# Performance work log

Measured on AMD Instinct MI355X. Metric: run time of the kernel, lower is better.

## Reference

```python
import jax, jax.numpy as jnp
import numpy as np

B, H, W, Z = 4, 256, 256, 64
ITERATIONS = 8
EPSILON = 1e-06
CENTER = 6.0  # 7-point Laplacian diagonal


def _stencil(x):
    # x: [B, H, W, Z]; zero (Dirichlet) boundaries via padded shifts
    west = jnp.pad(x[:, :, :-1, :], ((0, 0), (0, 0), (1, 0), (0, 0)))
    east = jnp.pad(x[:, :, 1:, :], ((0, 0), (0, 0), (0, 1), (0, 0)))
    north = jnp.pad(x[:, :-1, :, :], ((0, 0), (1, 0), (0, 0), (0, 0)))
    south = jnp.pad(x[:, 1:, :, :], ((0, 0), (0, 1), (0, 0), (0, 0)))
    bottom = jnp.pad(x[:, :, :, :-1], ((0, 0), (0, 0), (0, 0), (1, 0)))
    top = jnp.pad(x[:, :, :, 1:], ((0, 0), (0, 0), (0, 0), (0, 1)))
    return CENTER * x - west - east - south - north - bottom - top


def _dot(a, b):
    # per-sample dot product, keepdims for scalar broadcast
    return jnp.sum(a * b, axis=(1, 2, 3), keepdims=True)


def setup_inputs() -> dict:
    key = jax.random.key(0)
    k1, k2, k3 = jax.random.split(key, 3)
    shape = (B, H, W, Z)
    return {
        "x": jax.random.normal(k1, shape, dtype=jnp.float32),
        "b": jax.random.normal(k2, shape, dtype=jnp.float32),
        "reference_sol": jax.random.normal(k3, shape, dtype=jnp.float32),
    }


def reference(x, b, reference_sol):
    r = b - _stencil(x)
    p = r
    rho = _dot(r, r)

    def body(carry, _):
        x, r, p, rho = carry
        w = _stencil(p)
        eta = _dot(p, w)
        alpha = rho / (eta + EPSILON)
        x = x + alpha * p
        r = r - alpha * w
        rho_next = _dot(r, r)
        beta = rho_next / (rho + EPSILON)
        p = r + beta * p
        return (x, r, p, rho_next), None

    (x, r, p, rho), _ = jax.lax.scan(body, (x, r, p, rho), None, length=ITERATIONS)

    diff = x - reference_sol
    loss = jnp.mean(diff * diff)
    max_error = jnp.max(jnp.abs(diff))
    residual_norm_sq = jnp.mean(rho)
    return (loss, x, max_error, residual_norm_sq)
```

## Files before the change

### kernel.cpp

```cpp
#include <hip/hip_runtime.h>

#define B_ 4
#define H_ 256
#define W_ 256
#define Z_ 64
#define NB_ (H_*W_*Z_)
#define N_  (B_*NB_)
#define ITER_ 8
#define EPS_ 1e-6f
#define SLOTS_ 64

#define RHO_OFF   0
#define ETA_OFF   ((ITER_+1)*B_*SLOTS_)
#define LOSS_OFF  (ETA_OFF + ITER_*B_*SLOTS_)
#define MAXE_OFF  (LOSS_OFF + SLOTS_)
#define SCAL_FLOATS (MAXE_OFF + SLOTS_)

struct F8 { float4 a, b; };

__device__ __forceinline__ float wsum(float v){
  v += __shfl_xor(v,32); v += __shfl_xor(v,16); v += __shfl_xor(v,8);
  v += __shfl_xor(v,4);  v += __shfl_xor(v,2);  v += __shfl_xor(v,1);
  return v;
}
__device__ __forceinline__ float wmaxr(float v){
  v = fmaxf(v,__shfl_xor(v,32)); v = fmaxf(v,__shfl_xor(v,16));
  v = fmaxf(v,__shfl_xor(v,8));  v = fmaxf(v,__shfl_xor(v,4));
  v = fmaxf(v,__shfl_xor(v,2));  v = fmaxf(v,__shfl_xor(v,1));
  return v;
}
__device__ __forceinline__ float read_sum(const float* s){
  return wsum(s[threadIdx.x & 63]);
}
__device__ __forceinline__ void block_atomic_sum(float v, float* dst, float* lds){
  v = wsum(v);
  int wid = threadIdx.x >> 6, lane = threadIdx.x & 63;
  if (lane == 0) lds[wid] = v;
  __syncthreads();
  if (threadIdx.x == 0) atomicAdd(dst, lds[0]+lds[1]+lds[2]+lds[3]);
}

__device__ __forceinline__ float4 ld4(const float* p){ return *(const float4*)p; }

__device__ __forceinline__ void sub8(F8& s, const F8& n){
  s.a.x-=n.a.x; s.a.y-=n.a.y; s.a.z-=n.a.z; s.a.w-=n.a.w;
  s.b.x-=n.b.x; s.b.y-=n.b.y; s.b.z-=n.b.z; s.b.w-=n.b.w;
}

__device__ __forceinline__ void zcore(const F8& c, int zc, F8& st){
  float zl = __shfl_up(c.b.w, 1);
  float zr = __shfl_down(c.a.x, 1);
  zl = (zc > 0) ? zl : 0.f;
  zr = (zc < 7) ? zr : 0.f;
  st.a.x = 6.f*c.a.x - zl    - c.a.y;
  st.a.y = 6.f*c.a.y - c.a.x - c.a.z;
  st.a.z = 6.f*c.a.z - c.a.y - c.a.w;
  st.a.w = 6.f*c.a.w - c.a.z - c.b.x;
  st.b.x = 6.f*c.b.x - c.a.w - c.b.y;
  st.b.y = 6.f*c.b.y - c.b.x - c.b.z;
  st.b.z = 6.f*c.b.z - c.b.y - c.b.w;
  st.b.w = 6.f*c.b.w - c.b.z - zr;
}

__device__ __forceinline__ void stencil1_2(const float* __restrict__ a, int base0,
                                           int w, int h0, int zc,
                                           F8& c0, F8& c1, F8& st0, F8& st1)
{
  const int base1 = base0 + W_*Z_;
  c0.a = ld4(a+base0); c0.b = ld4(a+base0+4);
  c1.a = ld4(a+base1); c1.b = ld4(a+base1+4);
  zcore(c0, zc, st0);
  zcore(c1, zc, st1);
  F8 t;
  if (w > 0)    { t.a = ld4(a+base0-Z_); t.b = ld4(a+base0-Z_+4); sub8(st0,t);
                  t.a = ld4(a+base1-Z_); t.b = ld4(a+base1-Z_+4); sub8(st1,t); }
  if (w < W_-1) { t.a = ld4(a+base0+Z_); t.b = ld4(a+base0+Z_+4); sub8(st0,t);
                  t.a = ld4(a+base1+Z_); t.b = ld4(a+base1+Z_+4); sub8(st1,t); }
  if (h0 > 0)   { t.a = ld4(a+base0-W_*Z_); t.b = ld4(a+base0-W_*Z_+4); sub8(st0,t); }
  sub8(st0, c1);
  sub8(st1, c0);
  if (h0 < H_-2){ t.a = ld4(a+base1+W_*Z_); t.b = ld4(a+base1+W_*Z_+4); sub8(st1,t); }
}

__device__ __forceinline__ F8 comb8(const float* r, const float* p, float beta, int idx){
  F8 o;
  float4 ra = ld4(r+idx), rb = ld4(r+idx+4);
  float4 pa = ld4(p+idx), pb = ld4(p+idx+4);
  o.a.x = ra.x + beta*pa.x; o.a.y = ra.y + beta*pa.y;
  o.a.z = ra.z + beta*pa.z; o.a.w = ra.w + beta*pa.w;
  o.b.x = rb.x + beta*pb.x; o.b.y = rb.y + beta*pb.y;
  o.b.z = rb.z + beta*pb.z; o.b.w = rb.w + beta*pb.w;
  return o;
}
__device__ __forceinline__ void stencil2_2(const float* __restrict__ r,
                                           const float* __restrict__ p, float beta,
                                           int base0, int w, int h0, int zc,
                                           F8& c0, F8& c1, F8& st0, F8& st1)
{
  const int base1 = base0 + W_*Z_;
  c0 = comb8(r,p,beta,base0);
  c1 = comb8(r,p,beta,base1);
  zcore(c0, zc, st0);
  zcore(c1, zc, st1);
  if (w > 0)    { sub8(st0, comb8(r,p,beta,base0-Z_));
                  sub8(st1, comb8(r,p,beta,base1-Z_)); }
  if (w < W_-1) { sub8(st0, comb8(r,p,beta,base0+Z_));
                  sub8(st1, comb8(r,p,beta,base1+Z_)); }
  if (h0 > 0)   sub8(st0, comb8(r,p,beta,base0-W_*Z_));
  sub8(st0, c1);
  sub8(st1, c0);
  if (h0 < H_-2) sub8(st1, comb8(r,p,beta,base1+W_*Z_));
}

__device__ __forceinline__ float dot8(const F8& a, const F8& b){
  return a.a.x*b.a.x + a.a.y*b.a.y + a.a.z*b.a.z + a.a.w*b.a.w
       + a.b.x*b.b.x + a.b.y*b.b.y + a.b.z*b.b.z + a.b.w*b.b.w;
}

#define IDX2_SETUP \
  const int zc = threadIdx.x & 7; \
  const int wl = threadIdx.x >> 3; \
  const int w  = blockIdx.x*32 + wl; \
  const int h0 = blockIdx.y*2; \
  const int bb = blockIdx.z; \
  const int base0 = ((bb*H_ + h0)*W_ + w)*Z_ + zc*8; \
  const int flat = (blockIdx.z*gridDim.y + blockIdx.y)*gridDim.x + blockIdx.x; \
  const int slot = flat & (SLOTS_-1);

__global__ __launch_bounds__(256) void k_init2(const float* __restrict__ x,
                                               const float* __restrict__ b,
                                               float* __restrict__ r,
                                               float* scal)
{
  __shared__ float lds[4];
  IDX2_SETUP
  const int base1 = base0 + W_*Z_;
  F8 c0,c1,st0,st1;
  stencil1_2(x, base0, w, h0, zc, c0, c1, st0, st1);
  float4 b0 = ld4(b+base0), b1 = ld4(b+base0+4);
  float4 b2 = ld4(b+base1), b3 = ld4(b+base1+4);
  F8 rv0, rv1;
  rv0.a = make_float4(b0.x-st0.a.x, b0.y-st0.a.y, b0.z-st0.a.z, b0.w-st0.a.w);
  rv0.b = make_float4(b1.x-st0.b.x, b1.y-st0.b.y, b1.z-st0.b.z, b1.w-st0.b.w);
  rv1.a = make_float4(b2.x-st1.a.x, b2.y-st1.a.y, b2.z-st1.a.z, b2.w-st1.a.w);
  rv1.b = make_float4(b3.x-st1.b.x, b3.y-st1.b.y, b3.z-st1.b.z, b3.w-st1.b.w);
  *(float4*)(r+base0)   = rv0.a;
  *(float4*)(r+base0+4) = rv0.b;
  *(float4*)(r+base1)   = rv1.a;
  *(float4*)(r+base1+4) = rv1.b;
  block_atomic_sum(dot8(rv0,rv0)+dot8(rv1,rv1),
                   scal + RHO_OFF + (0*B_+bb)*SLOTS_ + slot, lds);
}

__global__ __launch_bounds__(256) void k_a0_2(const float* __restrict__ r,
                                              float* __restrict__ pnew,
                                              float* scal)
{
  __shared__ float lds[4];
  IDX2_SETUP
  const int base1 = base0 + W_*Z_;
  F8 c0,c1,st0,st1;
  stencil1_2(r, base0, w, h0, zc, c0, c1, st0, st1);
  if (pnew) {
    *(float4*)(pnew+base0)   = c0.a; *(float4*)(pnew+base0+4) = c0.b;
    *(float4*)(pnew+base1)   = c1.a; *(float4*)(pnew+base1+4) = c1.b;
  }
  block_atomic_sum(dot8(c0,st0)+dot8(c1,st1),
                   scal + ETA_OFF + (0*B_+bb)*SLOTS_ + slot, lds);
}

__global__ __launch_bounds__(256) void k_a2(const float* __restrict__ r,
                                            const float* __restrict__ pold,
                                            float* __restrict__ pnew,
                                            float* scal, int it)
{
  __shared__ float lds[4];
  IDX2_SETUP
  const int base1 = base0 + W_*Z_;
  float num = read_sum(scal + RHO_OFF + (it*B_+bb)*SLOTS_);
  float den = read_sum(scal + RHO_OFF + ((it-1)*B_+bb)*SLOTS_);
  float beta = num / (den + EPS_);
  F8 c0,c1,st0,st1;
  stencil2_2(r, pold, beta, base0, w, h0, zc, c0, c1, st0, st1);
  *(float4*)(pnew+base0)   = c0.a;
  *(float4*)(pnew+base0+4) = c0.b;
  *(float4*)(pnew+base1)   = c1.a;
  *(float4*)(pnew+base1+4) = c1.b;
  block_atomic_sum(dot8(c0,st0)+dot8(c1,st1),
                   scal + ETA_OFF + (it*B_+bb)*SLOTS_ + slot, lds);
}

__global__ __launch_bounds__(256) void k_b2(float* __restrict__ x,
                                            const float* r_in,
                                            float* r_out,
                                            const float* p,
                                            float* scal, int it)
{
  __shared__ float lds[4];
  IDX2_SETUP
  const int base1 = base0 + W_*Z_;
  float num = read_sum(scal + RHO_OFF + (it*B_+bb)*SLOTS_);
  float den = read_sum(scal + ETA_OFF + (it*B_+bb)*SLOTS_);
  float alpha = num / (den + EPS_);
  F8 c0,c1,st0,st1;
  stencil1_2(p, base0, w, h0, zc, c0, c1, st0, st1);
  float rho = 0.f;
  {
    float4 x0 = ld4(x+base0), x1 = ld4(x+base0+4);
    x0.x += alpha*c0.a.x; x0.y += alpha*c0.a.y; x0.z += alpha*c0.a.z; x0.w += alpha*c0.a.w;
    x1.x += alpha*c0.b.x; x1.y += alpha*c0.b.y; x1.z += alpha*c0.b.z; x1.w += alpha*c0.b.w;
    *(float4*)(x+base0)   = x0;
    *(float4*)(x+base0+4) = x1;
    float4 r0 = ld4(r_in+base0), r1 = ld4(r_in+base0+4);
    r0.x -= alpha*st0.a.x; r0.y -= alpha*st0.a.y; r0.z -= alpha*st0.a.z; r0.w -= alpha*st0.a.w;
    r1.x -= alpha*st0.b.x; r1.y -= alpha*st0.b.y; r1.z -= alpha*st0.b.z; r1.w -= alpha*st0.b.w;
    *(float4*)(r_out+base0)   = r0;
    *(float4*)(r_out+base0+4) = r1;
    rho += r0.x*r0.x + r0.y*r0.y + r0.z*r0.z + r0.w*r0.w
         + r1.x*r1.x + r1.y*r1.y + r1.z*r1.z + r1.w*r1.w;
  }
  {
    float4 x0 = ld4(x+base1), x1 = ld4(x+base1+4);
    x0.x += alpha*c1.a.x; x0.y += alpha*c1.a.y; x0.z += alpha*c1.a.z; x0.w += alpha*c1.a.w;
    x1.x += alpha*c1.b.x; x1.y += alpha*c1.b.y; x1.z += alpha*c1.b.z; x1.w += alpha*c1.b.w;
    *(float4*)(x+base1)   = x0;
    *(float4*)(x+base1+4) = x1;
    float4 r0 = ld4(r_in+base1), r1 = ld4(r_in+base1+4);
    r0.x -= alpha*st1.a.x; r0.y -= alpha*st1.a.y; r0.z -= alpha*st1.a.z; r0.w -= alpha*st1.a.w;
    r1.x -= alpha*st1.b.x; r1.y -= alpha*st1.b.y; r1.z -= alpha*st1.b.z; r1.w -= alpha*st1.b.w;
    *(float4*)(r_out+base1)   = r0;
    *(float4*)(r_out+base1+4) = r1;
    rho += r0.x*r0.x + r0.y*r0.y + r0.z*r0.z + r0.w*r0.w
         + r1.x*r1.x + r1.y*r1.y + r1.z*r1.z + r1.w*r1.w;
  }
  block_atomic_sum(rho, scal + RHO_OFF + ((it+1)*B_+bb)*SLOTS_ + slot, lds);
}

__device__ __forceinline__ void sten_core_o(const F8& c, const F8& wm, const F8& wp,
                                            const F8& hm, const F8& hp,
                                            float zl, float zr, F8& st)
{
  st.a.x = 6.f*c.a.x - wm.a.x - wp.a.x - hm.a.x - hp.a.x - zl     - c.a.y;
  st.a.y = 6.f*c.a.y - wm.a.y - wp.a.y - hm.a.y - hp.a.y - c.a.x  - c.a.z;
  st.a.z = 6.f*c.a.z - wm.a.z - wp.a.z - hm.a.z - hp.a.z - c.a.y  - c.a.w;
  st.a.w = 6.f*c.a.w - wm.a.w - wp.a.w - hm.a.w - hp.a.w - c.a.z  - c.b.x;
  st.b.x = 6.f*c.b.x - wm.b.x - wp.b.x - hm.b.x - hp.b.x - c.a.w  - c.b.y;
  st.b.y = 6.f*c.b.y - wm.b.y - wp.b.y - hm.b.y - hp.b.y - c.b.x  - c.b.z;
  st.b.z = 6.f*c.b.z - wm.b.z - wp.b.z - hm.b.z - hp.b.z - c.b.y  - c.b.w;
  st.b.w = 6.f*c.b.w - wm.b.w - wp.b.w - hm.b.w - hp.b.w - c.b.z  - zr;
}
__device__ __forceinline__ void stencil1_o(const float* __restrict__ a, int base,
                                           int w, int h, int zc, F8& c, F8& st)
{
  c.a = ld4(a+base); c.b = ld4(a+base+4);
  F8 zero; zero.a = make_float4(0,0,0,0); zero.b = zero.a;
  F8 wm = zero, wp = zero, hm = zero, hp = zero;
  if (w > 0)    { wm.a = ld4(a+base-Z_);    wm.b = ld4(a+base-Z_+4); }
  if (w < W_-1) { wp.a = ld4(a+base+Z_);    wp.b = ld4(a+base+Z_+4); }
  if (h > 0)    { hm.a = ld4(a+base-W_*Z_); hm.b = ld4(a+base-W_*Z_+4); }
  if (h < H_-1) { hp.a = ld4(a+base+W_*Z_); hp.b = ld4(a+base+W_*Z_+4); }
  float zl = (zc > 0) ? a[base-1] : 0.f;
  float zr = (zc < 7) ? a[base+8] : 0.f;
  sten_core_o(c, wm, wp, hm, hp, zl, zr, st);
}

__global__ __launch_bounds__(256) void k_b_fin(const float* __restrict__ x,
                                               const float* __restrict__ r,
                                               const float* __restrict__ p,
                                               const float* __restrict__ ref,
                                               float* __restrict__ out,
                                               float* scal, int it)
{
  __shared__ float xs[2048];
  __shared__ float lds[12];
  const int zc = threadIdx.x & 7;
  const int wl = threadIdx.x >> 3;
  const int w  = blockIdx.x*32 + wl;
  const int h  = blockIdx.y;
  const int bb = blockIdx.z;
  const int base = ((bb*H_ + h)*W_ + w)*Z_ + zc*8;
  const int flat = (blockIdx.z*gridDim.y + blockIdx.y)*gridDim.x + blockIdx.x;
  const int slot = flat & (SLOTS_-1);
  float num = read_sum(scal + RHO_OFF + (it*B_+bb)*SLOTS_);
  float den = read_sum(scal + ETA_OFF + (it*B_+bb)*SLOTS_);
  float alpha = num / (den + EPS_);
  F8 c, st;
  stencil1_o(p, base, w, h, zc, c, st);
  float4 x0 = ld4(x+base), x1 = ld4(x+base+4);
  x0.x += alpha*c.a.x; x0.y += alpha*c.a.y; x0.z += alpha*c.a.z; x0.w += alpha*c.a.w;
  x1.x += alpha*c.b.x; x1.y += alpha*c.b.y; x1.z += alpha*c.b.z; x1.w += alpha*c.b.w;
  float4 r0 = ld4(r+base), r1 = ld4(r+base+4);
  r0.x -= alpha*st.a.x; r0.y -= alpha*st.a.y; r0.z -= alpha*st.a.z; r0.w -= alpha*st.a.w;
  r1.x -= alpha*st.b.x; r1.y -= alpha*st.b.y; r1.z -= alpha*st.b.z; r1.w -= alpha*st.b.w;
  float rho = r0.x*r0.x + r0.y*r0.y + r0.z*r0.z + r0.w*r0.w
            + r1.x*r1.x + r1.y*r1.y + r1.z*r1.z + r1.w*r1.w;

  const int t = threadIdx.x;
  xs[t*8+0] = x0.x; xs[t*8+1] = x0.y; xs[t*8+2] = x0.z; xs[t*8+3] = x0.w;
  xs[t*8+4] = x1.x; xs[t*8+5] = x1.y; xs[t*8+6] = x1.z; xs[t*8+7] = x1.w;

  float4 f0 = ld4(ref+base), f1 = ld4(ref+base+4);
  float d0 = x0.x-f0.x, d1 = x0.y-f0.y, d2 = x0.z-f0.z, d3 = x0.w-f0.w;
  float d4 = x1.x-f1.x, d5 = x1.y-f1.y, d6 = x1.z-f1.z, d7 = x1.w-f1.w;
  float loss = d0*d0+d1*d1+d2*d2+d3*d3+d4*d4+d5*d5+d6*d6+d7*d7;
  float me = fmaxf(fmaxf(fmaxf(fabsf(d0),fabsf(d1)),fmaxf(fabsf(d2),fabsf(d3))),
                   fmaxf(fmaxf(fabsf(d4),fabsf(d5)),fmaxf(fabsf(d6),fabsf(d7))));

  float rs = wsum(rho), ls = wsum(loss), ms = wmaxr(me);
  int wid = t >> 6, lane = t & 63;
  if (lane == 0) { lds[wid] = rs; lds[4+wid] = ls; lds[8+wid] = ms; }
  __syncthreads();
  if (t == 0) {
    atomicAdd(scal + RHO_OFF + ((it+1)*B_+bb)*SLOTS_ + slot, lds[0]+lds[1]+lds[2]+lds[3]);
    atomicAdd(scal + LOSS_OFF + slot, lds[4]+lds[5]+lds[6]+lds[7]);
    float bm = fmaxf(fmaxf(lds[8],lds[9]), fmaxf(lds[10],lds[11]));
    atomicMax((unsigned int*)(scal + MAXE_OFF) + slot, __float_as_uint(bm));
  }

  const int S = flat * 2048;
  #pragma unroll
  for (int c2 = 0; c2 < 2; ++c2) {
    int q = t + 256*c2;
    if (q < 511) {
      float4 v = make_float4(xs[3+4*q], xs[4+4*q], xs[5+4*q], xs[6+4*q]);
      *(float4*)(out + S + 4 + 4*q) = v;
    } else if (q == 511) {
      out[S+1] = xs[0]; out[S+2] = xs[1]; out[S+3] = xs[2];
      out[S+2048] = xs[2047];
    }
  }
}

__global__ __launch_bounds__(64) void k_scal(const float* scal, float* out)
{
  int lane = threadIdx.x;
  float loss = wsum(scal[LOSS_OFF + lane]);
  float me   = wmaxr(__uint_as_float(((const unsigned int*)scal)[MAXE_OFF + lane]));
  float rho_sum = 0.f;
  for (int bb = 0; bb < B_; ++bb)
    rho_sum += wsum(scal[RHO_OFF + (ITER_*B_+bb)*SLOTS_ + lane]);
  if (lane == 0) {
    out[0]      = loss / (float)N_;
    out[1+N_]   = me;
    out[2+N_]   = rho_sum / (float)B_;
  }
}

extern "C" void kernel_launch(void* const* d_in, const int* in_sizes, int n_in,
                              void* d_out, int out_size, void* d_ws, size_t ws_size,
                              hipStream_t stream) {
  float* x         = (float*)d_in[0];
  const float* bv  = (const float*)d_in[1];
  const float* ref = (const float*)d_in[2];
  float* out       = (float*)d_out;
  float* ws        = (float*)d_ws;

  dim3 g2(W_/32, H_/2, B_), gF(W_/32, H_, B_), blk(256);
  bool fast = ws_size >= ((size_t)3*N_ + SCAL_FLOATS) * sizeof(float);

  if (fast) {
    float* R0 = ws;
    float* R1 = ws + N_;
    float* P0 = ws + 2*(size_t)N_;
    float* P1 = out;
    float* scal = ws + 3*(size_t)N_;
    (void)hipMemsetAsync(scal, 0, SCAL_FLOATS*sizeof(float), stream);

    k_init2<<<g2, blk, 0, stream>>>(x, bv, R0, scal);
    k_a0_2 <<<g2, blk, 0, stream>>>(R0, nullptr, scal);
    k_b2   <<<g2, blk, 0, stream>>>(x, R0, R1, R0, scal, 0);
    float* pa = P0; float* pb = R0;
    for (int it = 1; it < ITER_; ++it) {
      k_a2<<<g2, blk, 0, stream>>>(R1, pb, pa, scal, it);
      if (it < ITER_-1)
        k_b2<<<g2, blk, 0, stream>>>(x, R1, R1, pa, scal, it);
      else
        k_b_fin<<<gF, blk, 0, stream>>>(x, R1, pa, ref, out, scal, it);
      pb = pa; pa = (pa == P0) ? P1 : P0;
    }
  } else {
    float* r    = ws;
    float* p0w  = ws + N_;
    float* scal = ws + 2*(size_t)N_;
    (void)hipMemsetAsync(scal, 0, SCAL_FLOATS*sizeof(float), stream);

    k_init2<<<g2, blk, 0, stream>>>(x, bv, r, scal);
    k_a0_2 <<<g2, blk, 0, stream>>>(r, out, scal);
    k_b2   <<<g2, blk, 0, stream>>>(x, r, r, out, scal, 0);
    float* pa = p0w; float* pb = out;
    for (int it = 1; it < ITER_; ++it) {
      k_a2<<<g2, blk, 0, stream>>>(r, pb, pa, scal, it);
      if (it < ITER_-1)
        k_b2<<<g2, blk, 0, stream>>>(x, r, r, pa, scal, it);
      else
        k_b_fin<<<gF, blk, 0, stream>>>(x, r, pa, ref, out, scal, it);
      pb = pa; pa = (pa == p0w) ? out : p0w;
    }
  }
  k_scal<<<1, 64, 0, stream>>>((fast ? ws + 3*(size_t)N_ : ws + 2*(size_t)N_), out);
}
```

Before: 972.7 us.

## Defer x updates to every other iteration and fuse paired p contributions

The x update is deferred: even iterations skip reading and writing x, and odd iterations apply both the previous and current alpha*p terms in one pass, reading the older p buffer. The final kernel is also rewritten to process two h-rows per block, which folds in any pending x update. This lowers x read/write traffic on half the iterations at the cost of an extra p read, and requires the p buffers to stay alive one iteration longer, so P1 now reuses R0 instead of the output buffer.

```diff
diff --git a/kernel.cpp b/kernel.cpp
--- a/kernel.cpp
+++ b/kernel.cpp
@@ -190,6 +190,202 @@
                    scal + ETA_OFF + (it*B_+bb)*SLOTS_ + slot, lds);
 }
 
+__global__ __launch_bounds__(256) void k_b2_nox(const float* r_in,
+                                                float* r_out,
+                                                const float* p,
+                                                float* scal, int it)
+{
+  __shared__ float lds[4];
+  IDX2_SETUP
+  const int base1 = base0 + W_*Z_;
+  float num = read_sum(scal + RHO_OFF + (it*B_+bb)*SLOTS_);
+  float den = read_sum(scal + ETA_OFF + (it*B_+bb)*SLOTS_);
+  float alpha = num / (den + EPS_);
+  F8 c0,c1,st0,st1;
+  stencil1_2(p, base0, w, h0, zc, c0, c1, st0, st1);
+  float rho = 0.f;
+  {
+    float4 r0 = ld4(r_in+base0), r1 = ld4(r_in+base0+4);
+    r0.x -= alpha*st0.a.x; r0.y -= alpha*st0.a.y; r0.z -= alpha*st0.a.z; r0.w -= alpha*st0.a.w;
+    r1.x -= alpha*st0.b.x; r1.y -= alpha*st0.b.y; r1.z -= alpha*st0.b.z; r1.w -= alpha*st0.b.w;
+    *(float4*)(r_out+base0)   = r0;
+    *(float4*)(r_out+base0+4) = r1;
+    rho += r0.x*r0.x + r0.y*r0.y + r0.z*r0.z + r0.w*r0.w
+         + r1.x*r1.x + r1.y*r1.y + r1.z*r1.z + r1.w*r1.w;
+  }
+  {
+    float4 r0 = ld4(r_in+base1), r1 = ld4(r_in+base1+4);
+    r0.x -= alpha*st1.a.x; r0.y -= alpha*st1.a.y; r0.z -= alpha*st1.a.z; r0.w -= alpha*st1.a.w;
+    r1.x -= alpha*st1.b.x; r1.y -= alpha*st1.b.y; r1.z -= alpha*st1.b.z; r1.w -= alpha*st1.b.w;
+    *(float4*)(r_out+base1)   = r0;
+    *(float4*)(r_out+base1+4) = r1;
+    rho += r0.x*r0.x + r0.y*r0.y + r0.z*r0.z + r0.w*r0.w
+         + r1.x*r1.x + r1.y*r1.y + r1.z*r1.z + r1.w*r1.w;
+  }
+  block_atomic_sum(rho, scal + RHO_OFF + ((it+1)*B_+bb)*SLOTS_ + slot, lds);
+}
+
+__global__ __launch_bounds__(256) void k_b2_pair(float* __restrict__ x,
+                                                 const float* r_in,
+                                                 float* r_out,
+                                                 const float* p,
+                                                 const float* __restrict__ pprev,
+                                                 float* scal, int it)
+{
+  __shared__ float lds[4];
+  IDX2_SETUP
+  const int base1 = base0 + W_*Z_;
+  float num = read_sum(scal + RHO_OFF + (it*B_+bb)*SLOTS_);
+  float den = read_sum(scal + ETA_OFF + (it*B_+bb)*SLOTS_);
+  float alpha = num / (den + EPS_);
+  float nump = read_sum(scal + RHO_OFF + ((it-1)*B_+bb)*SLOTS_);
+  float denp = read_sum(scal + ETA_OFF + ((it-1)*B_+bb)*SLOTS_);
+  float alphap = nump / (denp + EPS_);
+  F8 c0,c1,st0,st1;
+  stencil1_2(p, base0, w, h0, zc, c0, c1, st0, st1);
+  float rho = 0.f;
+  {
+    float4 q0 = ld4(pprev+base0), q1 = ld4(pprev+base0+4);
+    float4 x0 = ld4(x+base0), x1 = ld4(x+base0+4);
+    x0.x += alphap*q0.x + alpha*c0.a.x; x0.y += alphap*q0.y + alpha*c0.a.y;
+    x0.z += alphap*q0.z + alpha*c0.a.z; x0.w += alphap*q0.w + alpha*c0.a.w;
+    x1.x += alphap*q1.x + alpha*c0.b.x; x1.y += alphap*q1.y + alpha*c0.b.y;
+    x1.z += alphap*q1.z + alpha*c0.b.z; x1.w += alphap*q1.w + alpha*c0.b.w;
+    *(float4*)(x+base0)   = x0;
+    *(float4*)(x+base0+4) = x1;
+    float4 r0 = ld4(r_in+base0), r1 = ld4(r_in+base0+4);
+    r0.x -= alpha*st0.a.x; r0.y -= alpha*st0.a.y; r0.z -= alpha*st0.a.z; r0.w -= alpha*st0.a.w;
+    r1.x -= alpha*st0.b.x; r1.y -= alpha*st0.b.y; r1.z -= alpha*st0.b.z; r1.w -= alpha*st0.b.w;
+    *(float4*)(r_out+base0)   = r0;
+    *(float4*)(r_out+base0+4) = r1;
+    rho += r0.x*r0.x + r0.y*r0.y + r0.z*r0.z + r0.w*r0.w
+         + r1.x*r1.x + r1.y*r1.y + r1.z*r1.z + r1.w*r1.w;
+  }
+  {
+    float4 q0 = ld4(pprev+base1), q1 = ld4(pprev+base1+4);
+    float4 x0 = ld4(x+base1), x1 = ld4(x+base1+4);
+    x0.x += alphap*q0.x + alpha*c1.a.x; x0.y += alphap*q0.y + alpha*c1.a.y;
+    x0.z += alphap*q0.z + alpha*c1.a.z; x0.w += alphap*q0.w + alpha*c1.a.w;
+    x1.x += alphap*q1.x + alpha*c1.b.x; x1.y += alphap*q1.y + alpha*c1.b.y;
+    x1.z += alphap*q1.z + alpha*c1.b.z; x1.w += alphap*q1.w + alpha*c1.b.w;
+    *(float4*)(x+base1)   = x0;
+    *(float4*)(x+base1+4) = x1;
+    float4 r0 = ld4(r_in+base1), r1 = ld4(r_in+base1+4);
+    r0.x -= alpha*st1.a.x; r0.y -= alpha*st1.a.y; r0.z -= alpha*st1.a.z; r0.w -= alpha*st1.a.w;
+    r1.x -= alpha*st1.b.x; r1.y -= alpha*st1.b.y; r1.z -= alpha*st1.b.z; r1.w -= alpha*st1.b.w;
+    *(float4*)(r_out+base1)   = r0;
+    *(float4*)(r_out+base1+4) = r1;
+    rho += r0.x*r0.x + r0.y*r0.y + r0.z*r0.z + r0.w*r0.w
+         + r1.x*r1.x + r1.y*r1.y + r1.z*r1.z + r1.w*r1.w;
+  }
+  block_atomic_sum(rho, scal + RHO_OFF + ((it+1)*B_+bb)*SLOTS_ + slot, lds);
+}
+
+__global__ __launch_bounds__(256) void k_fin2(const float* __restrict__ x,
+                                              const float* __restrict__ r,
+                                              const float* __restrict__ p,
+                                              const float* pprev,
+                                              const float* __restrict__ ref,
+                                              float* __restrict__ out,
+                                              float* scal, int it)
+{
+  __shared__ float xs[4096];
+  __shared__ float lds[12];
+  IDX2_SETUP
+  const int base1 = base0 + W_*Z_;
+  const int t = threadIdx.x;
+  float num = read_sum(scal + RHO_OFF + (it*B_+bb)*SLOTS_);
+  float den = read_sum(scal + ETA_OFF + (it*B_+bb)*SLOTS_);
+  float alpha = num / (den + EPS_);
+  float alphap = 0.f;
+  if (pprev) {
+    float nump = read_sum(scal + RHO_OFF + ((it-1)*B_+bb)*SLOTS_);
+    float denp = read_sum(scal + ETA_OFF + ((it-1)*B_+bb)*SLOTS_);
+    alphap = nump / (denp + EPS_);
+  }
+  F8 c0,c1,st0,st1;
+  stencil1_2(p, base0, w, h0, zc, c0, c1, st0, st1);
+
+  float rho = 0.f, loss = 0.f, me = 0.f;
+  float4 xa0, xa1, xb0, xb1;
+  {
+    xa0 = ld4(x+base0); xa1 = ld4(x+base0+4);
+    if (pprev) {
+      float4 q0 = ld4(pprev+base0), q1 = ld4(pprev+base0+4);
+      xa0.x += alphap*q0.x; xa0.y += alphap*q0.y; xa0.z += alphap*q0.z; xa0.w += alphap*q0.w;
+      xa1.x += alphap*q1.x; xa1.y += alphap*q1.y; xa1.z += alphap*q1.z; xa1.w += alphap*q1.w;
+    }
+    xa0.x += alpha*c0.a.x; xa0.y += alpha*c0.a.y; xa0.z += alpha*c0.a.z; xa0.w += alpha*c0.a.w;
+    xa1.x += alpha*c0.b.x; xa1.y += alpha*c0.b.y; xa1.z += alpha*c0.b.z; xa1.w += alpha*c0.b.w;
+    float4 r0 = ld4(r+base0), r1 = ld4(r+base0+4);
+    r0.x -= alpha*st0.a.x; r0.y -= alpha*st0.a.y; r0.z -= alpha*st0.a.z; r0.w -= alpha*st0.a.w;
+    r1.x -= alpha*st0.b.x; r1.y -= alpha*st0.b.y; r1.z -= alpha*st0.b.z; r1.w -= alpha*st0.b.w;
+    rho += r0.x*r0.x + r0.y*r0.y + r0.z*r0.z + r0.w*r0.w
+         + r1.x*r1.x + r1.y*r1.y + r1.z*r1.z + r1.w*r1.w;
+    float4 f0 = ld4(ref+base0), f1 = ld4(ref+base0+4);
+    float d0 = xa0.x-f0.x, d1 = xa0.y-f0.y, d2 = xa0.z-f0.z, d3 = xa0.w-f0.w;
+    float d4 = xa1.x-f1.x, d5 = xa1.y-f1.y, d6 = xa1.z-f1.z, d7 = xa1.w-f1.w;
+    loss += d0*d0+d1*d1+d2*d2+d3*d3+d4*d4+d5*d5+d6*d6+d7*d7;
+    me = fmaxf(me, fmaxf(fmaxf(fmaxf(fabsf(d0),fabsf(d1)),fmaxf(fabsf(d2),fabsf(d3))),
+                         fmaxf(fmaxf(fabsf(d4),fabsf(d5)),fmaxf(fabsf(d6),fabsf(d7)))));
+  }
+  {
+    xb0 = ld4(x+base1); xb1 = ld4(x+base1+4);
+    if (pprev) {
+      float4 q0 = ld4(pprev+base1), q1 = ld4(pprev+base1+4);
+      xb0.x += alphap*q0.x; xb0.y += alphap*q0.y; xb0.z += alphap*q0.z; xb0.w += alphap*q0.w;
+      xb1.x += alphap*q1.x; xb1.y += alphap*q1.y; xb1.z += alphap*q1.z; xb1.w += alphap*q1.w;
+    }
+    xb0.x += alpha*c1.a.x; xb0.y += alpha*c1.a.y; xb0.z += alpha*c1.a.z; xb0.w += alpha*c1.a.w;
+    xb1.x += alpha*c1.b.x; xb1.y += alpha*c1.b.y; xb1.z += alpha*c1.b.z; xb1.w += alpha*c1.b.w;
+    float4 r0 = ld4(r+base1), r1 = ld4(r+base1+4);
+    r0.x -= alpha*st1.a.x; r0.y -= alpha*st1.a.y; r0.z -= alpha*st1.a.z; r0.w -= alpha*st1.a.w;
+    r1.x -= alpha*st1.b.x; r1.y -= alpha*st1.b.y; r1.z -= alpha*st1.b.z; r1.w -= alpha*st1.b.w;
+    rho += r0.x*r0.x + r0.y*r0.y + r0.z*r0.z + r0.w*r0.w
+         + r1.x*r1.x + r1.y*r1.y + r1.z*r1.z + r1.w*r1.w;
+    float4 f0 = ld4(ref+base1), f1 = ld4(ref+base1+4);
+    float d0 = xb0.x-f0.x, d1 = xb0.y-f0.y, d2 = xb0.z-f0.z, d3 = xb0.w-f0.w;
+    float d4 = xb1.x-f1.x, d5 = xb1.y-f1.y, d6 = xb1.z-f1.z, d7 = xb1.w-f1.w;
+    loss += d0*d0+d1*d1+d2*d2+d3*d3+d4*d4+d5*d5+d6*d6+d7*d7;
+    me = fmaxf(me, fmaxf(fmaxf(fmaxf(fabsf(d0),fabsf(d1)),fmaxf(fabsf(d2),fabsf(d3))),
+                         fmaxf(fmaxf(fabsf(d4),fabsf(d5)),fmaxf(fabsf(d6),fabsf(d7)))));
+  }
+
+  xs[t*8+0] = xa0.x; xs[t*8+1] = xa0.y; xs[t*8+2] = xa0.z; xs[t*8+3] = xa0.w;
+  xs[t*8+4] = xa1.x; xs[t*8+5] = xa1.y; xs[t*8+6] = xa1.z; xs[t*8+7] = xa1.w;
+  xs[2048+t*8+0] = xb0.x; xs[2048+t*8+1] = xb0.y; xs[2048+t*8+2] = xb0.z; xs[2048+t*8+3] = xb0.w;
+  xs[2048+t*8+4] = xb1.x; xs[2048+t*8+5] = xb1.y; xs[2048+t*8+6] = xb1.z; xs[2048+t*8+7] = xb1.w;
+
+  float rs = wsum(rho), ls = wsum(loss), ms = wmaxr(me);
+  int wid = t >> 6, lane = t & 63;
+  if (lane == 0) { lds[wid] = rs; lds[4+wid] = ls; lds[8+wid] = ms; }
+  __syncthreads();
+  if (t == 0) {
+    atomicAdd(scal + RHO_OFF + ((it+1)*B_+bb)*SLOTS_ + slot, lds[0]+lds[1]+lds[2]+lds[3]);
+    atomicAdd(scal + LOSS_OFF + slot, lds[4]+lds[5]+lds[6]+lds[7]);
+    float bm = fmaxf(fmaxf(lds[8],lds[9]), fmaxf(lds[10],lds[11]));
+    atomicMax((unsigned int*)(scal + MAXE_OFF) + slot, __float_as_uint(bm));
+  }
+
+  const int S0 = ((bb*H_ + h0)*8 + (int)blockIdx.x)*2048;
+  #pragma unroll
+  for (int rr = 0; rr < 2; ++rr) {
+    const float* xr = xs + rr*2048;
+    const int S = S0 + rr*(8*2048);
+    #pragma unroll
+    for (int c2 = 0; c2 < 2; ++c2) {
+      int q = t + 256*c2;
+      if (q < 511) {
+        float4 v = make_float4(xr[3+4*q], xr[4+4*q], xr[5+4*q], xr[6+4*q]);
+        *(float4*)(out + S + 4 + 4*q) = v;
+      } else if (q == 511) {
+        out[S+1] = xr[0]; out[S+2] = xr[1]; out[S+3] = xr[2];
+        out[S+2048] = xr[2047];
+      }
+    }
+  }
+}
+
 __global__ __launch_bounds__(256) void k_b2(float* __restrict__ x,
                                             const float* r_in,
                                             float* r_out,
@@ -236,101 +432,6 @@
   block_atomic_sum(rho, scal + RHO_OFF + ((it+1)*B_+bb)*SLOTS_ + slot, lds);
 }
 
-__device__ __forceinline__ void sten_core_o(const F8& c, const F8& wm, const F8& wp,
-                                            const F8& hm, const F8& hp,
-                                            float zl, float zr, F8& st)
-{
-  st.a.x = 6.f*c.a.x - wm.a.x - wp.a.x - hm.a.x - hp.a.x - zl     - c.a.y;
-  st.a.y = 6.f*c.a.y - wm.a.y - wp.a.y - hm.a.y - hp.a.y - c.a.x  - c.a.z;
-  st.a.z = 6.f*c.a.z - wm.a.z - wp.a.z - hm.a.z - hp.a.z - c.a.y  - c.a.w;
-  st.a.w = 6.f*c.a.w - wm.a.w - wp.a.w - hm.a.w - hp.a.w - c.a.z  - c.b.x;
-  st.b.x = 6.f*c.b.x - wm.b.x - wp.b.x - hm.b.x - hp.b.x - c.a.w  - c.b.y;
-  st.b.y = 6.f*c.b.y - wm.b.y - wp.b.y - hm.b.y - hp.b.y - c.b.x  - c.b.z;
-  st.b.z = 6.f*c.b.z - wm.b.z - wp.b.z - hm.b.z - hp.b.z - c.b.y  - c.b.w;
-  st.b.w = 6.f*c.b.w - wm.b.w - wp.b.w - hm.b.w - hp.b.w - c.b.z  - zr;
-}
-__device__ __forceinline__ void stencil1_o(const float* __restrict__ a, int base,
-                                           int w, int h, int zc, F8& c, F8& st)
-{
-  c.a = ld4(a+base); c.b = ld4(a+base+4);
-  F8 zero; zero.a = make_float4(0,0,0,0); zero.b = zero.a;
-  F8 wm = zero, wp = zero, hm = zero, hp = zero;
-  if (w > 0)    { wm.a = ld4(a+base-Z_);    wm.b = ld4(a+base-Z_+4); }
-  if (w < W_-1) { wp.a = ld4(a+base+Z_);    wp.b = ld4(a+base+Z_+4); }
-  if (h > 0)    { hm.a = ld4(a+base-W_*Z_); hm.b = ld4(a+base-W_*Z_+4); }
-  if (h < H_-1) { hp.a = ld4(a+base+W_*Z_); hp.b = ld4(a+base+W_*Z_+4); }
-  float zl = (zc > 0) ? a[base-1] : 0.f;
-  float zr = (zc < 7) ? a[base+8] : 0.f;
-  sten_core_o(c, wm, wp, hm, hp, zl, zr, st);
-}
-
-__global__ __launch_bounds__(256) void k_b_fin(const float* __restrict__ x,
-                                               const float* __restrict__ r,
-                                               const float* __restrict__ p,
-                                               const float* __restrict__ ref,
-                                               float* __restrict__ out,
-                                               float* scal, int it)
-{
-  __shared__ float xs[2048];
-  __shared__ float lds[12];
-  const int zc = threadIdx.x & 7;
-  const int wl = threadIdx.x >> 3;
-  const int w  = blockIdx.x*32 + wl;
-  const int h  = blockIdx.y;
-  const int bb = blockIdx.z;
-  const int base = ((bb*H_ + h)*W_ + w)*Z_ + zc*8;
-  const int flat = (blockIdx.z*gridDim.y + blockIdx.y)*gridDim.x + blockIdx.x;
-  const int slot = flat & (SLOTS_-1);
-  float num = read_sum(scal + RHO_OFF + (it*B_+bb)*SLOTS_);
-  float den = read_sum(scal + ETA_OFF + (it*B_+bb)*SLOTS_);
-  float alpha = num / (den + EPS_);
-  F8 c, st;
-  stencil1_o(p, base, w, h, zc, c, st);
-  float4 x0 = ld4(x+base), x1 = ld4(x+base+4);
-  x0.x += alpha*c.a.x; x0.y += alpha*c.a.y; x0.z += alpha*c.a.z; x0.w += alpha*c.a.w;
-  x1.x += alpha*c.b.x; x1.y += alpha*c.b.y; x1.z += alpha*c.b.z; x1.w += alpha*c.b.w;
-  float4 r0 = ld4(r+base), r1 = ld4(r+base+4);
-  r0.x -= alpha*st.a.x; r0.y -= alpha*st.a.y; r0.z -= alpha*st.a.z; r0.w -= alpha*st.a.w;
-  r1.x -= alpha*st.b.x; r1.y -= alpha*st.b.y; r1.z -= alpha*st.b.z; r1.w -= alpha*st.b.w;
-  float rho = r0.x*r0.x + r0.y*r0.y + r0.z*r0.z + r0.w*r0.w
-            + r1.x*r1.x + r1.y*r1.y + r1.z*r1.z + r1.w*r1.w;
-
-  const int t = threadIdx.x;
-  xs[t*8+0] = x0.x; xs[t*8+1] = x0.y; xs[t*8+2] = x0.z; xs[t*8+3] = x0.w;
-  xs[t*8+4] = x1.x; xs[t*8+5] = x1.y; xs[t*8+6] = x1.z; xs[t*8+7] = x1.w;
-
-  float4 f0 = ld4(ref+base), f1 = ld4(ref+base+4);
-  float d0 = x0.x-f0.x, d1 = x0.y-f0.y, d2 = x0.z-f0.z, d3 = x0.w-f0.w;
-  float d4 = x1.x-f1.x, d5 = x1.y-f1.y, d6 = x1.z-f1.z, d7 = x1.w-f1.w;
-  float loss = d0*d0+d1*d1+d2*d2+d3*d3+d4*d4+d5*d5+d6*d6+d7*d7;
-  float me = fmaxf(fmaxf(fmaxf(fabsf(d0),fabsf(d1)),fmaxf(fabsf(d2),fabsf(d3))),
-                   fmaxf(fmaxf(fabsf(d4),fabsf(d5)),fmaxf(fabsf(d6),fabsf(d7))));
-
-  float rs = wsum(rho), ls = wsum(loss), ms = wmaxr(me);
-  int wid = t >> 6, lane = t & 63;
-  if (lane == 0) { lds[wid] = rs; lds[4+wid] = ls; lds[8+wid] = ms; }
-  __syncthreads();
-  if (t == 0) {
-    atomicAdd(scal + RHO_OFF + ((it+1)*B_+bb)*SLOTS_ + slot, lds[0]+lds[1]+lds[2]+lds[3]);
-    atomicAdd(scal + LOSS_OFF + slot, lds[4]+lds[5]+lds[6]+lds[7]);
-    float bm = fmaxf(fmaxf(lds[8],lds[9]), fmaxf(lds[10],lds[11]));
-    atomicMax((unsigned int*)(scal + MAXE_OFF) + slot, __float_as_uint(bm));
-  }
-
-  const int S = flat * 2048;
-  #pragma unroll
-  for (int c2 = 0; c2 < 2; ++c2) {
-    int q = t + 256*c2;
-    if (q < 511) {
-      float4 v = make_float4(xs[3+4*q], xs[4+4*q], xs[5+4*q], xs[6+4*q]);
-      *(float4*)(out + S + 4 + 4*q) = v;
-    } else if (q == 511) {
-      out[S+1] = xs[0]; out[S+2] = xs[1]; out[S+3] = xs[2];
-      out[S+2048] = xs[2047];
-    }
-  }
-}
-
 __global__ __launch_bounds__(64) void k_scal(const float* scal, float* out)
 {
   int lane = threadIdx.x;
@@ -355,33 +456,35 @@
   float* out       = (float*)d_out;
   float* ws        = (float*)d_ws;
 
-  dim3 g2(W_/32, H_/2, B_), gF(W_/32, H_, B_), blk(256);
+  dim3 g2(W_/32, H_/2, B_), blk(256);
   bool fast = ws_size >= ((size_t)3*N_ + SCAL_FLOATS) * sizeof(float);
+  float* scal;
 
   if (fast) {
     float* R0 = ws;
     float* R1 = ws + N_;
     float* P0 = ws + 2*(size_t)N_;
-    float* P1 = out;
-    float* scal = ws + 3*(size_t)N_;
+    scal = ws + 3*(size_t)N_;
     (void)hipMemsetAsync(scal, 0, SCAL_FLOATS*sizeof(float), stream);
 
-    k_init2<<<g2, blk, 0, stream>>>(x, bv, R0, scal);
-    k_a0_2 <<<g2, blk, 0, stream>>>(R0, nullptr, scal);
-    k_b2   <<<g2, blk, 0, stream>>>(x, R0, R1, R0, scal, 0);
-    float* pa = P0; float* pb = R0;
+    k_init2 <<<g2, blk, 0, stream>>>(x, bv, R0, scal);
+    k_a0_2  <<<g2, blk, 0, stream>>>(R0, nullptr, scal);
+    k_b2_nox<<<g2, blk, 0, stream>>>(R0, R1, R0, scal, 0);
     for (int it = 1; it < ITER_; ++it) {
-      k_a2<<<g2, blk, 0, stream>>>(R1, pb, pa, scal, it);
-      if (it < ITER_-1)
-        k_b2<<<g2, blk, 0, stream>>>(x, R1, R1, pa, scal, it);
+      float* pnew = (it & 1) ? P0 : R0;
+      float* pold = (it & 1) ? R0 : P0;
+      k_a2<<<g2, blk, 0, stream>>>(R1, pold, pnew, scal, it);
+      if (it == ITER_-1)
+        k_fin2<<<g2, blk, 0, stream>>>(x, R1, pnew, pold, ref, out, scal, it);
+      else if (it & 1)
+        k_b2_pair<<<g2, blk, 0, stream>>>(x, R1, R1, pnew, pold, scal, it);
       else
-        k_b_fin<<<gF, blk, 0, stream>>>(x, R1, pa, ref, out, scal, it);
-      pb = pa; pa = (pa == P0) ? P1 : P0;
+        k_b2_nox<<<g2, blk, 0, stream>>>(R1, R1, pnew, scal, it);
     }
   } else {
     float* r    = ws;
     float* p0w  = ws + N_;
-    float* scal = ws + 2*(size_t)N_;
+    scal = ws + 2*(size_t)N_;
     (void)hipMemsetAsync(scal, 0, SCAL_FLOATS*sizeof(float), stream);
 
     k_init2<<<g2, blk, 0, stream>>>(x, bv, r, scal);
@@ -393,9 +496,9 @@
       if (it < ITER_-1)
         k_b2<<<g2, blk, 0, stream>>>(x, r, r, pa, scal, it);
       else
-        k_b_fin<<<gF, blk, 0, stream>>>(x, r, pa, ref, out, scal, it);
+        k_fin2<<<g2, blk, 0, stream>>>(x, r, pa, nullptr, ref, out, scal, it);
       pb = pa; pa = (pa == p0w) ? out : p0w;
     }
   }
-  k_scal<<<1, 64, 0, stream>>>((fast ? ws + 3*(size_t)N_ : ws + 2*(size_t)N_), out);
-}
+  k_scal<<<1, 64, 0, stream>>>(scal, out);
+}
```

New measurement: 943.1 us. 3.0% less time.
